# Optimization experiments

Hardware: AMD Instinct MI355X
Metric: run time of the kernel (lower is better)

The kernel has to match this reference:

```python
import jax, jax.numpy as jnp
import numpy as np

B, T = 4, 8192
C = 64            # dilation_channels (also embedding size)
S = 256           # skip_dims
V = 256           # waveform_categories (8-bit mu-law)
CENTER = 128      # waveform_center_cat
DILATIONS = [1, 2, 4, 8, 16, 32, 64, 128, 256, 512] * 3  # 3 blocks, 30 layers
L = len(DILATIONS)


def setup_inputs() -> dict:
    key = jax.random.key(0)
    ks = jax.random.split(key, 16)
    waveform = jax.random.randint(ks[0], (B, T, 1), 0, V, dtype=jnp.int32)
    waveform_lens = jax.random.randint(ks[1], (B,), 0, T, dtype=jnp.int32)
    s = 0.05
    embed = jax.random.normal(ks[2], (V, C), dtype=jnp.float32) * s
    # conv_w[l, 0] applies to x[t-d], conv_w[l, 1] to x[t] (kernel_size=2)
    conv_w = jax.random.normal(ks[3], (L, 2, C, 2 * C), dtype=jnp.float32) * s
    conv_b = jnp.zeros((L, 2 * C), dtype=jnp.float32)
    res_w = jax.random.normal(ks[4], (L, C, C), dtype=jnp.float32) * s
    res_b = jnp.zeros((L, C), dtype=jnp.float32)
    skip_w = jax.random.normal(ks[5], (L, C, S), dtype=jnp.float32) * s
    skip_b = jnp.zeros((L, S), dtype=jnp.float32)
    w0 = jax.random.normal(ks[6], (S, V), dtype=jnp.float32) * s
    b0 = jnp.zeros((V,), dtype=jnp.float32)
    w1 = jax.random.normal(ks[7], (V, V), dtype=jnp.float32) * s
    b1 = jnp.zeros((V,), dtype=jnp.float32)
    return dict(waveform=waveform, waveform_lens=waveform_lens, embed=embed,
                conv_w=conv_w, conv_b=conv_b, res_w=res_w, res_b=res_b,
                skip_w=skip_w, skip_b=skip_b, w0=w0, b0=b0, w1=w1, b1=b1)


def _wavenet(wf, lens, embed, conv_w, conv_b, res_w, res_b, skip_w, skip_b, w0, b0, w1, b1):
    labels = wf[..., 0]                                          # (B, T) int
    # shift right with <go> = center category
    inp = jnp.concatenate(
        [jnp.full((B, 1), CENTER, dtype=labels.dtype), labels[:, :-1]], axis=1)
    x = embed[inp]                                               # (B, T, C)
    skip_sum = jnp.zeros((B, T, S), dtype=x.dtype)
    for i, d in enumerate(DILATIONS):
        # dilated causal conv, kernel 2: y[t] = x[t-d] @ W0 + x[t] @ W1 + b
        x_shift = jnp.pad(x, ((0, 0), (d, 0), (0, 0)))[:, :T]    # left pad d
        h = (jnp.einsum('btc,cf->btf', x_shift, conv_w[i, 0])
             + jnp.einsum('btc,cf->btf', x, conv_w[i, 1]) + conv_b[i])
        gate = jnp.tanh(h[..., :C]) * jax.nn.sigmoid(h[..., C:])  # (B, T, C)
        x = x + jnp.einsum('btc,cd->btd', gate, res_w[i]) + res_b[i]
        skip_sum = skip_sum + jnp.einsum('btc,cs->bts', gate, skip_w[i]) + skip_b[i]
    hid0 = jax.nn.relu(jnp.einsum('bts,sv->btv', skip_sum, w0) + b0)
    logits = jnp.einsum('btv,vu->btu', hid0, w1) + b1            # (B, T, V)
    logp = jax.nn.log_softmax(logits, axis=-1)
    ce = -jnp.take_along_axis(logp, labels[..., None], axis=-1)[..., 0]  # (B, T)
    mask = (jnp.arange(T)[None, :] < lens[:, None]).astype(logits.dtype)
    loss = jnp.sum(ce * mask) / jnp.maximum(jnp.sum(mask), 1.0)
    return loss


def reference(waveform, waveform_lens, embed, conv_w, conv_b, res_w, res_b,
              skip_w, skip_b, w0, b0, w1, b1):
    return _wavenet(waveform, waveform_lens, embed, conv_w, conv_b, res_w,
                    res_b, skip_w, skip_b, w0, b0, w1, b1)
```

## Files before the change

### kernel.cpp

```cpp
#include <hip/hip_runtime.h>

#define NB 4
#define NT 8192
#define NC 64
#define NS 256
#define NV 256
#define NL 30

typedef __attribute__((ext_vector_type(8))) short bf16x8;
typedef __attribute__((ext_vector_type(4))) float f32x4;
typedef unsigned short ushort_t;

#define MFMA(a, b, c) __builtin_amdgcn_mfma_f32_16x16x32_bf16(a, b, c, 0, 0, 0)

#define OFF_WCAT 0
#define SZ_WCAT  (NL * 16384)
#define OFF_RW   (OFF_WCAT + SZ_WCAT)
#define SZ_RW    (NL * 4096)
#define OFF_SWG  (OFF_RW + SZ_RW)
#define SZ_SWG   (6 * 81920)
#define OFF_W0   (OFF_SWG + SZ_SWG)
#define OFF_W1   (OFF_W0 + 65536)
#define TOTAL_W  (OFF_W1 + 65536)
#define N_PREP   (TOTAL_W + 1792)

#define X_ELEMS  (NB * NT * NC)
#define SK_ELEMS (NB * NT * NS)
#define G_ELEMS  (NB * NT * NC)

#define WS_SMALL ((size_t)(2 * X_ELEMS + SK_ELEMS + 5 * G_ELEMS + TOTAL_W) * 2 \
                  + 1792 * 4)
#define WS_BIG   ((size_t)(2 * X_ELEMS + 30 * G_ELEMS + TOTAL_W) * 2 + 1792 * 4)

__device__ inline ushort_t f2bu(float f) {
  union { float f; unsigned u; } v; v.f = f;
  unsigned r = v.u + 0x7FFFu + ((v.u >> 16) & 1u);
  return (ushort_t)(r >> 16);
}
__device__ inline float b2f(ushort_t h) {
  union { unsigned u; float f; } v; v.u = ((unsigned)h) << 16; return v.f;
}

__global__ void sentinel_kernel(float* __restrict__ out) {
  if (threadIdx.x == 0) out[0] = -1234.0f;
}

__global__ __launch_bounds__(256) void prep_kernel(
    const float* __restrict__ cw, const float* __restrict__ rw,
    const float* __restrict__ sw, const float* __restrict__ w0,
    const float* __restrict__ w1, const float* __restrict__ sb_all,
    ushort_t* __restrict__ wt, float* __restrict__ sbg,
    float* __restrict__ out0)
{
  int idx = blockIdx.x * 256 + threadIdx.x;
  if (idx == 0) out0[0] = 0.f;
  if (idx >= N_PREP) return;
  if (idx >= TOTAL_W) {
    int j = idx - TOTAL_W;
    if (j < 1536) {
      int g = j >> 8, n = j & 255;
      float s = 0.f;
#pragma unroll
      for (int jj = 0; jj < 5; ++jj) s += sb_all[(5 * g + jj) * 256 + n];
      sbg[j] = s;
    } else {
      int n = j - 1536;
      float s = 0.f;
      for (int jj = 0; jj < NL; ++jj) s += sb_all[jj * 256 + n];
      sbg[j] = s;
    }
    return;
  }
  float v;
  if (idx < OFF_RW) {
    int e = idx; int l = e >> 14; int r = e & 16383;
    int kk = r >> 12, n = (r >> 5) & 127, j = r & 31;
    int k = kk * 32 + j, tap = k >> 6, c = k & 63;
    v = cw[(((l * 2 + tap) << 6) + c) * 128 + n];
  } else if (idx < OFF_SWG) {
    int e = idx - OFF_RW; int l = e >> 12; int r = e & 4095;
    int kk = r >> 11, n = (r >> 5) & 63, j = r & 31;
    int k = kk * 32 + j;
    v = rw[((l << 6) + k) * 64 + n];
  } else if (idx < OFF_W0) {
    int e = idx - OFF_SWG; int g = e / 81920; int r = e % 81920;
    int kk = r >> 13; int rem = r & 8191;
    int n = rem >> 5, jj = rem & 31;
    int k = kk * 32 + jj;
    v = sw[(size_t)(320 * g + k) * 256 + n];
  } else if (idx < OFF_W1) {
    int e = idx - OFF_W0;
    int kk = e >> 13; int rem = e & 8191;
    int n = rem >> 5, jj = rem & 31;
    int k = kk * 32 + jj;
    v = w0[k * 256 + n];
  } else {
    int e = idx - OFF_W1;
    int kk = e >> 13; int rem = e & 8191;
    int n = rem >> 5, jj = rem & 31;
    int k = kk * 32 + jj;
    v = w1[k * 256 + n];
  }
  wt[idx] = f2bu(v);
}

__global__ __launch_bounds__(256) void embed_kernel(
    const int* __restrict__ wf, const float* __restrict__ embed,
    ushort_t* __restrict__ x0)
{
  const int bidx = blockIdx.x;
  const int bb = bidx >> 7;
  const int t0 = (bidx & 127) << 6;
  const int pos0 = bb * NT + t0;
  for (int e = threadIdx.x; e < 64 * 64; e += 256) {
    int p = e >> 6, c = e & 63;
    int t = t0 + p;
    int id = (t == 0) ? 128 : wf[bb * NT + t - 1];
    x0[(size_t)(pos0 + p) * NC + c] = f2bu(embed[id * NC + c]);
  }
}

__global__ __launch_bounds__(384) void chain5_kernel(
    const ushort_t* __restrict__ xin, ushort_t* __restrict__ xout,
    ushort_t* __restrict__ gates,
    const ushort_t* __restrict__ wt,
    const float* __restrict__ cb_all, const float* __restrict__ rb_all,
    int l0, const int* __restrict__ wf, const float* __restrict__ embf)
{
  __shared__ __align__(16) ushort_t xt[96][72];
  __shared__ __align__(16) ushort_t gt[96][72];

  const int tid = threadIdx.x;
  const int w = tid >> 6, lane = tid & 63;
  const int quad = lane >> 4, c16 = lane & 15;
  const int bb = blockIdx.x >> 7;
  const int t0 = (blockIdx.x & 127) << 6;
  const size_t row0 = (size_t)bb * NT;

#pragma unroll
  for (int i = 0; i < 2; ++i) {
    int e = tid + i * 384;
    int r = e >> 3, c0 = (e & 7) * 8;
    int t = t0 - 32 + r;
    bf16x8 v;
    if (t >= 0) {
      if (embf) {
        int id = (t == 0) ? 128 : wf[row0 + t - 1];
        const float* ep = embf + id * NC + c0;
#pragma unroll
        for (int jj = 0; jj < 8; ++jj) v[jj] = (short)f2bu(ep[jj]);
      } else {
        v = *(const bf16x8*)(xin + (row0 + t) * 64 + c0);
      }
    } else { bf16x8 z = {0, 0, 0, 0, 0, 0, 0, 0}; v = z; }
    *(bf16x8*)&xt[r][c0] = v;
  }
  __syncthreads();

  for (int j = 0; j < 5; ++j) {
    const int l = l0 + j;
    const int d = 1 << j;
    const ushort_t* wcat = wt + OFF_WCAT + l * 16384;
    const ushort_t* rww  = wt + OFF_RW + l * 4096;
    const float* cb = cb_all + l * 128;
    const float* rb = rb_all + l * 64;

    bf16x8 af[4];
    {
      int lr = w * 16 + c16;
#pragma unroll
      for (int kk = 0; kk < 4; ++kk) {
        int rr = (kk < 2) ? lr - d : lr;
        int ch = (kk & 1) * 32 + quad * 8;
        if (rr >= 0) af[kk] = *(const bf16x8*)&xt[rr][ch];
        else { bf16x8 z = {0, 0, 0, 0, 0, 0, 0, 0}; af[kk] = z; }
      }
    }
    __syncthreads();

    {
      f32x4 acc[8];
#pragma unroll
      for (int q = 0; q < 4; ++q) {
        float ba = cb[q * 16 + c16], bs = cb[q * 16 + c16 + 64];
        f32x4 va = {ba, ba, ba, ba}, vb = {bs, bs, bs, bs};
        acc[q] = va; acc[4 + q] = vb;
      }
#pragma unroll
      for (int kk = 0; kk < 4; ++kk) {
        const ushort_t* wp = wcat + kk * 4096 + c16 * 32 + quad * 8;
#pragma unroll
        for (int q = 0; q < 4; ++q) {
          acc[q]     = MFMA(af[kk], *(const bf16x8*)(wp + q * 512), acc[q]);
          acc[4 + q] = MFMA(af[kk], *(const bf16x8*)(wp + q * 512 + 2048), acc[4 + q]);
        }
      }
#pragma unroll
      for (int q = 0; q < 4; ++q)
#pragma unroll
        for (int r = 0; r < 4; ++r) {
          float e2 = __expf(2.f * acc[q][r]);
          float th = (e2 - 1.f) / (e2 + 1.f);
          float sg = 1.f / (1.f + __expf(-acc[4 + q][r]));
          gt[w * 16 + quad * 4 + r][q * 16 + c16] = f2bu(th * sg);
        }

      bf16x8 gf0 = *(const bf16x8*)&gt[w * 16 + c16][quad * 8];
      bf16x8 gf1 = *(const bf16x8*)&gt[w * 16 + c16][32 + quad * 8];

      f32x4 acc2[4];
#pragma unroll
      for (int q = 0; q < 4; ++q) {
        float bv = rb[q * 16 + c16];
        f32x4 z = {bv, bv, bv, bv};
        acc2[q] = z;
      }
      const ushort_t* wp2 = rww + c16 * 32 + quad * 8;
#pragma unroll
      for (int q = 0; q < 4; ++q)
        acc2[q] = MFMA(gf0, *(const bf16x8*)(wp2 + q * 512), acc2[q]);
#pragma unroll
      for (int q = 0; q < 4; ++q)
        acc2[q] = MFMA(gf1, *(const bf16x8*)(wp2 + q * 512 + 2048), acc2[q]);
#pragma unroll
      for (int q = 0; q < 4; ++q) {
        int n = q * 16 + c16;
#pragma unroll
        for (int r = 0; r < 4; ++r) {
          int rowi = w * 16 + quad * 4 + r;
          xt[rowi][n] = f2bu(b2f(xt[rowi][n]) + acc2[q][r]);
        }
      }
    }
    __syncthreads();

    {
      ushort_t* gslot = gates + (size_t)j * G_ELEMS;
      int e = tid;
      {
        int r = e >> 3, c0 = (e & 7) * 8;
        *(bf16x8*)(gslot + (row0 + t0 + r) * 64 + c0) =
            *(const bf16x8*)&gt[32 + r][c0];
      }
      e = tid + 384;
      if (e < 512) {
        int r = e >> 3, c0 = (e & 7) * 8;
        *(bf16x8*)(gslot + (row0 + t0 + r) * 64 + c0) =
            *(const bf16x8*)&gt[32 + r][c0];
      }
    }
  }
  __syncthreads();

  {
    int e = tid;
    {
      int r = e >> 3, c0 = (e & 7) * 8;
      *(bf16x8*)(xout + (row0 + t0 + r) * 64 + c0) = *(const bf16x8*)&xt[32 + r][c0];
    }
    e = tid + 384;
    if (e < 512) {
      int r = e >> 3, c0 = (e & 7) * 8;
      *(bf16x8*)(xout + (row0 + t0 + r) * 64 + c0) = *(const bf16x8*)&xt[32 + r][c0];
    }
  }
}

__global__ __launch_bounds__(384) void chain5hi_kernel(
    const ushort_t* __restrict__ xin, ushort_t* __restrict__ xout,
    ushort_t* __restrict__ gates,
    const ushort_t* __restrict__ wt,
    const float* __restrict__ cb_all, const float* __restrict__ rb_all,
    int lbase, int write_x)
{
  __shared__ __align__(16) ushort_t xt[96][72];
  __shared__ __align__(16) ushort_t gt[96][72];

  const int tid = threadIdx.x;
  const int w = tid >> 6, lane = tid & 63;
  const int quad = lane >> 4, c16 = lane & 15;
  const int bb = blockIdx.x >> 7;
  const int sub = blockIdx.x & 127;
  const int k = sub & 31;
  const int i0 = (sub >> 5) << 6;
  const size_t row0 = (size_t)bb * NT;

#pragma unroll
  for (int i = 0; i < 2; ++i) {
    int e = tid + i * 384;
    int r = e >> 3, c0 = (e & 7) * 8;
    int ii = i0 + r - 32;
    bf16x8 v;
    if (ii >= 0) v = *(const bf16x8*)(xin + (row0 + (size_t)ii * 32 + k) * 64 + c0);
    else { bf16x8 z = {0, 0, 0, 0, 0, 0, 0, 0}; v = z; }
    *(bf16x8*)&xt[r][c0] = v;
  }
  __syncthreads();

  for (int j = 0; j < 5; ++j) {
    const int l = lbase + j;
    const int d = 1 << j;
    const ushort_t* wcat = wt + OFF_WCAT + l * 16384;
    const ushort_t* rww  = wt + OFF_RW + l * 4096;
    const float* cb = cb_all + l * 128;
    const float* rb = rb_all + l * 64;

    bf16x8 af[4];
    {
      int lr = w * 16 + c16;
#pragma unroll
      for (int kk = 0; kk < 4; ++kk) {
        int rr = (kk < 2) ? lr - d : lr;
        int ch = (kk & 1) * 32 + quad * 8;
        if (rr >= 0) af[kk] = *(const bf16x8*)&xt[rr][ch];
        else { bf16x8 z = {0, 0, 0, 0, 0, 0, 0, 0}; af[kk] = z; }
      }
    }
    __syncthreads();

    {
      f32x4 acc[8];
#pragma unroll
      for (int q = 0; q < 4; ++q) {
        float ba = cb[q * 16 + c16], bs = cb[q * 16 + c16 + 64];
        f32x4 va = {ba, ba, ba, ba}, vb = {bs, bs, bs, bs};
        acc[q] = va; acc[4 + q] = vb;
      }
#pragma unroll
      for (int kk = 0; kk < 4; ++kk) {
        const ushort_t* wp = wcat + kk * 4096 + c16 * 32 + quad * 8;
#pragma unroll
        for (int q = 0; q < 4; ++q) {
          acc[q]     = MFMA(af[kk], *(const bf16x8*)(wp + q * 512), acc[q]);
          acc[4 + q] = MFMA(af[kk], *(const bf16x8*)(wp + q * 512 + 2048), acc[4 + q]);
        }
      }
#pragma unroll
      for (int q = 0; q < 4; ++q)
#pragma unroll
        for (int r = 0; r < 4; ++r) {
          float e2 = __expf(2.f * acc[q][r]);
          float th = (e2 - 1.f) / (e2 + 1.f);
          float sg = 1.f / (1.f + __expf(-acc[4 + q][r]));
          gt[w * 16 + quad * 4 + r][q * 16 + c16] = f2bu(th * sg);
        }

      if (write_x || j < 4) {
        bf16x8 gf0 = *(const bf16x8*)&gt[w * 16 + c16][quad * 8];
        bf16x8 gf1 = *(const bf16x8*)&gt[w * 16 + c16][32 + quad * 8];

        f32x4 acc2[4];
#pragma unroll
        for (int q = 0; q < 4; ++q) {
          float bv = rb[q * 16 + c16];
          f32x4 z = {bv, bv, bv, bv};
          acc2[q] = z;
        }
        const ushort_t* wp2 = rww + c16 * 32 + quad * 8;
#pragma unroll
        for (int q = 0; q < 4; ++q)
          acc2[q] = MFMA(gf0, *(const bf16x8*)(wp2 + q * 512), acc2[q]);
#pragma unroll
        for (int q = 0; q < 4; ++q)
          acc2[q] = MFMA(gf1, *(const bf16x8*)(wp2 + q * 512 + 2048), acc2[q]);
#pragma unroll
        for (int q = 0; q < 4; ++q) {
          int n = q * 16 + c16;
#pragma unroll
          for (int r = 0; r < 4; ++r) {
            int rowi = w * 16 + quad * 4 + r;
            xt[rowi][n] = f2bu(b2f(xt[rowi][n]) + acc2[q][r]);
          }
        }
      }
    }
    __syncthreads();

    {
      ushort_t* gslot = gates + (size_t)j * G_ELEMS;
      int e = tid;
      {
        int r = e >> 3, c0 = (e & 7) * 8;
        *(bf16x8*)(gslot + (row0 + (size_t)(i0 + r) * 32 + k) * 64 + c0) =
            *(const bf16x8*)&gt[32 + r][c0];
      }
      e = tid + 384;
      if (e < 512) {
        int r = e >> 3, c0 = (e & 7) * 8;
        *(bf16x8*)(gslot + (row0 + (size_t)(i0 + r) * 32 + k) * 64 + c0) =
            *(const bf16x8*)&gt[32 + r][c0];
      }
    }
  }
  __syncthreads();

  if (write_x) {
    int e = tid;
    {
      int r = e >> 3, c0 = (e & 7) * 8;
      *(bf16x8*)(xout + (row0 + (size_t)(i0 + r) * 32 + k) * 64 + c0) =
          *(const bf16x8*)&xt[32 + r][c0];
    }
    e = tid + 384;
    if (e < 512) {
      int r = e >> 3, c0 = (e & 7) * 8;
      *(bf16x8*)(xout + (row0 + (size_t)(i0 + r) * 32 + k) * 64 + c0) =
          *(const bf16x8*)&xt[32 + r][c0];
    }
  }
}

__global__ __launch_bounds__(256) void skip30_head_kernel(
    const ushort_t* __restrict__ gates,
    const ushort_t* __restrict__ wt,
    const float* __restrict__ sbtot,
    const float* __restrict__ b0, const float* __restrict__ b1,
    const int* __restrict__ wf, const int* __restrict__ lens,
    float* __restrict__ loss)
{
  __shared__ __align__(16) ushort_t wbuf[2][8192];
  __shared__ __align__(16) ushort_t tile[64][264];
  const int tid = threadIdx.x;
  const int w = tid >> 6, lane = tid & 63;
  const int quad = lane >> 4, c16 = lane & 15;
  const int bb = blockIdx.x >> 7;
  const int t0 = (blockIdx.x & 127) << 6;
  const int tb = t0 + w * 16;
  const size_t row0 = (size_t)bb * NT;
  const int mylen = lens[bb];
  const ushort_t* swg = wt + OFF_SWG;

  f32x4 acc[16];
#pragma unroll
  for (int nt = 0; nt < 16; ++nt) { f32x4 z = {0.f, 0.f, 0.f, 0.f}; acc[nt] = z; }

  const size_t arow = (row0 + tb + c16) * 64;
  bf16x8 wreg[4];
#pragma unroll
  for (int i = 0; i < 4; ++i)
    wreg[i] = ((const bf16x8*)swg)[tid + i * 256];
  bf16x8 af0 = *(const bf16x8*)(gates + arow + quad * 8);
  bf16x8 af1 = *(const bf16x8*)(gates + (size_t)0 * G_ELEMS + arow + 32 + quad * 8);
  int cur = 0;

  for (int kk = 0; kk < 60; ++kk) {
#pragma unroll
    for (int i = 0; i < 4; ++i)
      ((bf16x8*)wbuf[cur])[tid + i * 256] = wreg[i];
    int kn = (kk + 1 < 60) ? kk + 1 : 59;
#pragma unroll
    for (int i = 0; i < 4; ++i)
      wreg[i] = ((const bf16x8*)(swg + (size_t)kn * 8192))[tid + i * 256];
    int ka = (kk + 2 < 60) ? kk + 2 : 59;
    bf16x8 af2 = *(const bf16x8*)(gates + (size_t)(ka >> 1) * G_ELEMS + arow +
                                  (ka & 1) * 32 + quad * 8);
    __syncthreads();
    const ushort_t* wp = wbuf[cur] + c16 * 32 + quad * 8;
#pragma unroll
    for (int nt = 0; nt < 16; ++nt)
      acc[nt] = MFMA(af0, *(const bf16x8*)(wp + nt * 512), acc[nt]);
    af0 = af1; af1 = af2; cur ^= 1;
  }

#pragma unroll
  for (int nt = 0; nt < 16; ++nt) {
    int n = nt * 16 + c16;
    float sbn = sbtot[n];
#pragma unroll
    for (int r = 0; r < 4; ++r)
      tile[w * 16 + quad * 4 + r][n] = f2bu(acc[nt][r] + sbn);
  }

  const ushort_t* w0T = wt + OFF_W0;
  f32x4 accA[16];
#pragma unroll
  for (int nt = 0; nt < 16; ++nt) {
    float bv = b0[nt * 16 + c16];
    f32x4 z = {bv, bv, bv, bv};
    accA[nt] = z;
  }
  for (int kk = 0; kk < 8; ++kk) {
#pragma unroll
    for (int i = 0; i < 4; ++i)
      ((bf16x8*)wbuf[0])[tid + i * 256] = ((const bf16x8*)(w0T + kk * 8192))[tid + i * 256];
    __syncthreads();
    bf16x8 hf = *(const bf16x8*)&tile[w * 16 + c16][kk * 32 + quad * 8];
    const ushort_t* wp = wbuf[0] + c16 * 32 + quad * 8;
#pragma unroll
    for (int nt = 0; nt < 16; ++nt)
      accA[nt] = MFMA(hf, *(const bf16x8*)(wp + nt * 512), accA[nt]);
    __syncthreads();
  }
#pragma unroll
  for (int nt = 0; nt < 16; ++nt)
#pragma unroll
    for (int r = 0; r < 4; ++r)
      tile[w * 16 + quad * 4 + r][nt * 16 + c16] = f2bu(fmaxf(accA[nt][r], 0.f));

  const ushort_t* w1T = wt + OFF_W1;
  f32x4 acc2[16];
#pragma unroll
  for (int nt = 0; nt < 16; ++nt) {
    float bv = b1[nt * 16 + c16];
    f32x4 z = {bv, bv, bv, bv};
    acc2[nt] = z;
  }
  for (int kk = 0; kk < 8; ++kk) {
#pragma unroll
    for (int i = 0; i < 4; ++i)
      ((bf16x8*)wbuf[0])[tid + i * 256] = ((const bf16x8*)(w1T + kk * 8192))[tid + i * 256];
    __syncthreads();
    bf16x8 hf = *(const bf16x8*)&tile[w * 16 + c16][kk * 32 + quad * 8];
    const ushort_t* wp = wbuf[0] + c16 * 32 + quad * 8;
#pragma unroll
    for (int nt = 0; nt < 16; ++nt)
      acc2[nt] = MFMA(hf, *(const bf16x8*)(wp + nt * 512), acc2[nt]);
    __syncthreads();
  }

  int lblv[4];
#pragma unroll
  for (int r = 0; r < 4; ++r)
    lblv[r] = wf[row0 + tb + quad * 4 + r];

  float local = 0.f;
#pragma unroll
  for (int r = 0; r < 4; ++r) {
    float m = -1e30f, tv = -1e30f;
#pragma unroll
    for (int nt = 0; nt < 16; ++nt) {
      float v = acc2[nt][r];
      m = fmaxf(m, v);
      if (lblv[r] == nt * 16 + c16) tv = v;
    }
#pragma unroll
    for (int dd = 1; dd < 16; dd <<= 1) m = fmaxf(m, __shfl_xor(m, dd));
    float s = 0.f;
#pragma unroll
    for (int nt = 0; nt < 16; ++nt) s += __expf(acc2[nt][r] - m);
#pragma unroll
    for (int dd = 1; dd < 16; dd <<= 1) {
      s += __shfl_xor(s, dd);
      tv = fmaxf(tv, __shfl_xor(tv, dd));
    }
    int t = tb + quad * 4 + r;
    if (c16 == 0 && t < mylen) local += (m + __logf(s)) - tv;
  }
#pragma unroll
  for (int dd = 1; dd < 64; dd <<= 1) local += __shfl_xor(local, dd);
  if (lane == 0 && local != 0.f) atomicAdd(loss, local);
}

__global__ __launch_bounds__(256) void skip_kernel(
    ushort_t* __restrict__ skip, const ushort_t* __restrict__ gates,
    const ushort_t* __restrict__ swg, const float* __restrict__ sbg,
    int first)
{
  __shared__ __align__(16) ushort_t wbuf[8192];
  const int tid = threadIdx.x;
  const int w = tid >> 6, lane = tid & 63;
  const int quad = lane >> 4, c16 = lane & 15;
  const int bb = blockIdx.x >> 7;
  const int t0 = (blockIdx.x & 127) << 6;
  const int tb = t0 + w * 16;
  const size_t row0 = (size_t)bb * NT;

  f32x4 acc[16];
#pragma unroll
  for (int nt = 0; nt < 16; ++nt) { f32x4 z = {0.f, 0.f, 0.f, 0.f}; acc[nt] = z; }

  const size_t arow = (row0 + tb + c16) * 64;
  for (int kk = 0; kk < 10; ++kk) {
#pragma unroll
    for (int i = 0; i < 4; ++i)
      ((bf16x8*)wbuf)[tid + i * 256] = ((const bf16x8*)(swg + kk * 8192))[tid + i * 256];
    __syncthreads();

    int slot = kk >> 1;
    bf16x8 af = *(const bf16x8*)(gates + (size_t)slot * G_ELEMS + arow +
                                 (kk & 1) * 32 + quad * 8);
    const ushort_t* wp = wbuf + c16 * 32 + quad * 8;
#pragma unroll
    for (int nt = 0; nt < 16; ++nt)
      acc[nt] = MFMA(af, *(const bf16x8*)(wp + nt * 512), acc[nt]);
    __syncthreads();
  }

#pragma unroll
  for (int nt = 0; nt < 16; ++nt) {
    int n = nt * 16 + c16;
    float sbn = sbg[n];
#pragma unroll
    for (int r = 0; r < 4; ++r) {
      size_t idx = (row0 + tb + quad * 4 + r) * 256 + n;
      float old = first ? 0.f : b2f(skip[idx]);
      skip[idx] = f2bu(old + acc[nt][r] + sbn);
    }
  }
}

__global__ __launch_bounds__(256) void head_kernel(
    const ushort_t* __restrict__ skip,
    const ushort_t* __restrict__ w0T, const float* __restrict__ b0,
    const ushort_t* __restrict__ w1T, const float* __restrict__ b1,
    const int* __restrict__ wf, const int* __restrict__ lens,
    float* __restrict__ loss)
{
  __shared__ __align__(16) ushort_t wbuf[8192];
  __shared__ __align__(16) ushort_t tile[64][264];
  const int tid = threadIdx.x;
  const int w = tid >> 6, lane = tid & 63;
  const int quad = lane >> 4, c16 = lane & 15;
  const int bb = blockIdx.x >> 7;
  const int t0 = (blockIdx.x & 127) << 6;
  const int tb = t0 + w * 16;
  const size_t row0 = (size_t)bb * NT;
  const int mylen = lens[bb];

#pragma unroll
  for (int i = 0; i < 8; ++i) {
    int e = lane + i * 64;
    int r = e >> 5, c0 = (e & 31) * 8;
    *(bf16x8*)&tile[w * 16 + r][c0] =
        *(const bf16x8*)(skip + (row0 + t0 + w * 16 + r) * 256 + c0);
  }

  f32x4 accA[16];
#pragma unroll
  for (int nt = 0; nt < 16; ++nt) {
    float bv = b0[nt * 16 + c16];
    f32x4 z = {bv, bv, bv, bv};
    accA[nt] = z;
  }
  for (int kk = 0; kk < 8; ++kk) {
#pragma unroll
    for (int i = 0; i < 4; ++i)
      ((bf16x8*)wbuf)[tid + i * 256] = ((const bf16x8*)(w0T + kk * 8192))[tid + i * 256];
    __syncthreads();
    bf16x8 af = *(const bf16x8*)&tile[w * 16 + c16][kk * 32 + quad * 8];
    const ushort_t* wp = wbuf + c16 * 32 + quad * 8;
#pragma unroll
    for (int nt = 0; nt < 16; ++nt)
      accA[nt] = MFMA(af, *(const bf16x8*)(wp + nt * 512), accA[nt]);
    __syncthreads();
  }
#pragma unroll
  for (int nt = 0; nt < 16; ++nt)
#pragma unroll
    for (int r = 0; r < 4; ++r)
      tile[w * 16 + quad * 4 + r][nt * 16 + c16] = f2bu(fmaxf(accA[nt][r], 0.f));

  f32x4 acc2[16];
#pragma unroll
  for (int nt = 0; nt < 16; ++nt) {
    float bv = b1[nt * 16 + c16];
    f32x4 z = {bv, bv, bv, bv};
    acc2[nt] = z;
  }
  for (int kk = 0; kk < 8; ++kk) {
#pragma unroll
    for (int i = 0; i < 4; ++i)
      ((bf16x8*)wbuf)[tid + i * 256] = ((const bf16x8*)(w1T + kk * 8192))[tid + i * 256];
    __syncthreads();
    bf16x8 hf = *(const bf16x8*)&tile[w * 16 + c16][kk * 32 + quad * 8];
    const ushort_t* wp = wbuf + c16 * 32 + quad * 8;
#pragma unroll
    for (int nt = 0; nt < 16; ++nt)
      acc2[nt] = MFMA(hf, *(const bf16x8*)(wp + nt * 512), acc2[nt]);
    __syncthreads();
  }

  int lblv[4];
#pragma unroll
  for (int r = 0; r < 4; ++r)
    lblv[r] = wf[row0 + tb + quad * 4 + r];

  float local = 0.f;
#pragma unroll
  for (int r = 0; r < 4; ++r) {
    float m = -1e30f, tv = -1e30f;
#pragma unroll
    for (int nt = 0; nt < 16; ++nt) {
      float v = acc2[nt][r];
      m = fmaxf(m, v);
      if (lblv[r] == nt * 16 + c16) tv = v;
    }
#pragma unroll
    for (int dd = 1; dd < 16; dd <<= 1) m = fmaxf(m, __shfl_xor(m, dd));
    float s = 0.f;
#pragma unroll
    for (int nt = 0; nt < 16; ++nt) s += __expf(acc2[nt][r] - m);
#pragma unroll
    for (int dd = 1; dd < 16; dd <<= 1) {
      s += __shfl_xor(s, dd);
      tv = fmaxf(tv, __shfl_xor(tv, dd));
    }
    int t = tb + quad * 4 + r;
    if (c16 == 0 && t < mylen) local += (m + __logf(s)) - tv;
  }
#pragma unroll
  for (int dd = 1; dd < 64; dd <<= 1) local += __shfl_xor(local, dd);
  if (lane == 0 && local != 0.f) atomicAdd(loss, local);
}

__global__ void finalize_kernel(const int* __restrict__ lens,
                                float* __restrict__ out)
{
  if (threadIdx.x == 0) {
    float den = 0.f;
    for (int b = 0; b < NB; ++b) {
      int l = lens[b];
      if (l > NT) l = NT;
      den += (float)l;
    }
    out[0] = out[0] / fmaxf(den, 1.f);
  }
}

extern "C" void kernel_launch(void* const* d_in, const int* in_sizes, int n_in,
                              void* d_out, int out_size, void* d_ws, size_t ws_size,
                              hipStream_t stream) {
  const int*   wf     = (const int*)d_in[0];
  const int*   lens   = (const int*)d_in[1];
  const float* embed  = (const float*)d_in[2];
  const float* conv_w = (const float*)d_in[3];
  const float* conv_b = (const float*)d_in[4];
  const float* res_w  = (const float*)d_in[5];
  const float* res_b  = (const float*)d_in[6];
  const float* skip_w = (const float*)d_in[7];
  const float* skip_b = (const float*)d_in[8];
  const float* w0     = (const float*)d_in[9];
  const float* b0     = (const float*)d_in[10];
  const float* w1     = (const float*)d_in[11];
  const float* b1     = (const float*)d_in[12];

  float* out = (float*)d_out;
  if (ws_size < WS_SMALL) {
    sentinel_kernel<<<1, 64, 0, stream>>>(out);
    return;
  }
  const bool big = (ws_size >= WS_BIG);

  if (big) {
    ushort_t* x0    = (ushort_t*)d_ws;
    ushort_t* x1    = x0 + X_ELEMS;
    ushort_t* gates = x1 + X_ELEMS;
    ushort_t* wt    = gates + 30 * (size_t)G_ELEMS;
    float*    sbg   = (float*)(wt + TOTAL_W);

    prep_kernel<<<(N_PREP + 255) / 256, 256, 0, stream>>>(
        conv_w, res_w, skip_w, w0, w1, skip_b, wt, sbg, out);

    const ushort_t* xin = x0;
    ushort_t* xout = x1;
    for (int blk = 0; blk < 3; ++blk) {
      const int l0 = blk * 10;
      chain5_kernel<<<512, 384, 0, stream>>>(
          xin, xout, gates + (size_t)(2 * blk) * 5 * G_ELEMS,
          wt, conv_b, res_b, l0, wf, blk == 0 ? embed : nullptr);
      { const ushort_t* t = xout; xout = (ushort_t*)xin; xin = t; }
      chain5hi_kernel<<<512, 384, 0, stream>>>(
          xin, xout, gates + (size_t)(2 * blk + 1) * 5 * G_ELEMS,
          wt, conv_b, res_b, l0 + 5, blk < 2 ? 1 : 0);
      { const ushort_t* t = xout; xout = (ushort_t*)xin; xin = t; }
    }

    skip30_head_kernel<<<512, 256, 0, stream>>>(
        gates, wt, sbg + 1536, b0, b1, wf, lens, out);
    finalize_kernel<<<1, 64, 0, stream>>>(lens, out);
  } else {
    ushort_t* x0    = (ushort_t*)d_ws;
    ushort_t* x1    = x0 + X_ELEMS;
    ushort_t* skip  = x1 + X_ELEMS;
    ushort_t* gates = skip + SK_ELEMS;
    ushort_t* wt    = gates + 5 * (size_t)G_ELEMS;
    float*    sbg   = (float*)(wt + TOTAL_W);

    prep_kernel<<<(N_PREP + 255) / 256, 256, 0, stream>>>(
        conv_w, res_w, skip_w, w0, w1, skip_b, wt, sbg, out);
    embed_kernel<<<512, 256, 0, stream>>>(wf, embed, x0);

    const ushort_t* xin = x0;
    ushort_t* xout = x1;
    for (int blk = 0; blk < 3; ++blk) {
      const int l0 = blk * 10;
      chain5_kernel<<<512, 384, 0, stream>>>(
          xin, xout, gates, wt, conv_b, res_b, l0, wf, nullptr);
      { const ushort_t* t = xout; xout = (ushort_t*)xin; xin = t; }
      skip_kernel<<<512, 256, 0, stream>>>(
          skip, gates, wt + OFF_SWG + (size_t)(2 * blk) * 81920,
          sbg + (size_t)(2 * blk) * 256, blk == 0 ? 1 : 0);
      chain5hi_kernel<<<512, 384, 0, stream>>>(
          xin, xout, gates, wt, conv_b, res_b, l0 + 5, blk < 2 ? 1 : 0);
      { const ushort_t* t = xout; xout = (ushort_t*)xin; xin = t; }
      skip_kernel<<<512, 256, 0, stream>>>(
          skip, gates, wt + OFF_SWG + (size_t)(2 * blk + 1) * 81920,
          sbg + (size_t)(2 * blk + 1) * 256, 0);
    }

    head_kernel<<<512, 256, 0, stream>>>(
        skip, wt + OFF_W0, b0, wt + OFF_W1, b1, wf, lens, out);
    finalize_kernel<<<1, 64, 0, stream>>>(lens, out);
  }
}
```

Measured before the change: 431.0 us.

## Split skip GEMM by output columns per wave, reading weights directly from global

The skip-sum GEMM in the head kernel is re-tiled. Each wave now computes all 64 time rows for a 64-column slice of the 256 skip outputs, instead of 16 rows across all 256 columns. Weight fragments are read straight from global memory (L2) rather than staged through a double-buffered LDS buffer, which removes the per-iteration __syncthreads and LDS stores. The gate fragments are now loaded four times per wave from global, and the software prefetch of the next K slice is dropped, so memory latency may be exposed. LDS use falls with the single weight buffer.

Measured after the change: 463.3 us. 7.5% more time.

```diff
diff --git a/kernel.cpp b/kernel.cpp
--- a/kernel.cpp
+++ b/kernel.cpp
@@ -418,7 +418,7 @@
     const int* __restrict__ wf, const int* __restrict__ lens,
     float* __restrict__ loss)
 {
-  __shared__ __align__(16) ushort_t wbuf[2][8192];
+  __shared__ __align__(16) ushort_t wbuf[8192];
   __shared__ __align__(16) ushort_t tile[64][264];
   const int tid = threadIdx.x;
   const int w = tid >> 6, lane = tid & 63;
@@ -430,46 +430,41 @@
   const int mylen = lens[bb];
   const ushort_t* swg = wt + OFF_SWG;
 
-  f32x4 acc[16];
-#pragma unroll
-  for (int nt = 0; nt < 16; ++nt) { f32x4 z = {0.f, 0.f, 0.f, 0.f}; acc[nt] = z; }
-
-  const size_t arow = (row0 + tb + c16) * 64;
-  bf16x8 wreg[4];
-#pragma unroll
-  for (int i = 0; i < 4; ++i)
-    wreg[i] = ((const bf16x8*)swg)[tid + i * 256];
-  bf16x8 af0 = *(const bf16x8*)(gates + arow + quad * 8);
-  bf16x8 af1 = *(const bf16x8*)(gates + (size_t)0 * G_ELEMS + arow + 32 + quad * 8);
-  int cur = 0;
-
+  f32x4 acc[4][4];
+#pragma unroll
+  for (int m = 0; m < 4; ++m)
+#pragma unroll
+    for (int nt = 0; nt < 4; ++nt) { f32x4 z = {0.f, 0.f, 0.f, 0.f}; acc[m][nt] = z; }
+
+  const size_t arow = (row0 + t0 + c16) * 64;
   for (int kk = 0; kk < 60; ++kk) {
-#pragma unroll
-    for (int i = 0; i < 4; ++i)
-      ((bf16x8*)wbuf[cur])[tid + i * 256] = wreg[i];
-    int kn = (kk + 1 < 60) ? kk + 1 : 59;
-#pragma unroll
-    for (int i = 0; i < 4; ++i)
-      wreg[i] = ((const bf16x8*)(swg + (size_t)kn * 8192))[tid + i * 256];
-    int ka = (kk + 2 < 60) ? kk + 2 : 59;
-    bf16x8 af2 = *(const bf16x8*)(gates + (size_t)(ka >> 1) * G_ELEMS + arow +
-                                  (ka & 1) * 32 + quad * 8);
-    __syncthreads();
-    const ushort_t* wp = wbuf[cur] + c16 * 32 + quad * 8;
-#pragma unroll
-    for (int nt = 0; nt < 16; ++nt)
-      acc[nt] = MFMA(af0, *(const bf16x8*)(wp + nt * 512), acc[nt]);
-    af0 = af1; af1 = af2; cur ^= 1;
-  }
-
-#pragma unroll
-  for (int nt = 0; nt < 16; ++nt) {
-    int n = nt * 16 + c16;
-    float sbn = sbtot[n];
-#pragma unroll
-    for (int r = 0; r < 4; ++r)
-      tile[w * 16 + quad * 4 + r][n] = f2bu(acc[nt][r] + sbn);
-  }
+    const ushort_t* gslot = gates + (size_t)(kk >> 1) * G_ELEMS;
+    const int koff = (kk & 1) * 32 + quad * 8;
+    bf16x8 af[4];
+#pragma unroll
+    for (int m = 0; m < 4; ++m)
+      af[m] = *(const bf16x8*)(gslot + arow + (size_t)m * 1024 + koff);
+    const ushort_t* wp = swg + (size_t)kk * 8192 + w * 2048 + c16 * 32 + quad * 8;
+#pragma unroll
+    for (int nt = 0; nt < 4; ++nt) {
+      bf16x8 bfv = *(const bf16x8*)(wp + nt * 512);
+#pragma unroll
+      for (int m = 0; m < 4; ++m)
+        acc[m][nt] = MFMA(af[m], bfv, acc[m][nt]);
+    }
+  }
+
+#pragma unroll
+  for (int m = 0; m < 4; ++m)
+#pragma unroll
+    for (int nt = 0; nt < 4; ++nt) {
+      int n = w * 64 + nt * 16 + c16;
+      float sbn = sbtot[n];
+#pragma unroll
+      for (int r = 0; r < 4; ++r)
+        tile[m * 16 + quad * 4 + r][n] = f2bu(acc[m][nt][r] + sbn);
+    }
+  __syncthreads();
 
   const ushort_t* w0T = wt + OFF_W0;
   f32x4 accA[16];
@@ -482,10 +477,10 @@
   for (int kk = 0; kk < 8; ++kk) {
 #pragma unroll
     for (int i = 0; i < 4; ++i)
-      ((bf16x8*)wbuf[0])[tid + i * 256] = ((const bf16x8*)(w0T + kk * 8192))[tid + i * 256];
+      ((bf16x8*)wbuf)[tid + i * 256] = ((const bf16x8*)(w0T + kk * 8192))[tid + i * 256];
     __syncthreads();
     bf16x8 hf = *(const bf16x8*)&tile[w * 16 + c16][kk * 32 + quad * 8];
-    const ushort_t* wp = wbuf[0] + c16 * 32 + quad * 8;
+    const ushort_t* wp = wbuf + c16 * 32 + quad * 8;
 #pragma unroll
     for (int nt = 0; nt < 16; ++nt)
       accA[nt] = MFMA(hf, *(const bf16x8*)(wp + nt * 512), accA[nt]);
@@ -508,10 +503,10 @@
   for (int kk = 0; kk < 8; ++kk) {
 #pragma unroll
     for (int i = 0; i < 4; ++i)
-      ((bf16x8*)wbuf[0])[tid + i * 256] = ((const bf16x8*)(w1T + kk * 8192))[tid + i * 256];
+      ((bf16x8*)wbuf)[tid + i * 256] = ((const bf16x8*)(w1T + kk * 8192))[tid + i * 256];
     __syncthreads();
     bf16x8 hf = *(const bf16x8*)&tile[w * 16 + c16][kk * 32 + quad * 8];
-    const ushort_t* wp = wbuf[0] + c16 * 32 + quad * 8;
+    const ushort_t* wp = wbuf + c16 * 32 + quad * 8;
 #pragma unroll
     for (int nt = 0; nt < 16; ++nt)
       acc2[nt] = MFMA(hf, *(const bf16x8*)(wp + nt * 512), acc2[nt]);
```
